# Kernel tuning notes

Hardware: AMD Instinct MI355X
Metric: run time of the kernel (lower is better)

## Reference

```python
import jax, jax.numpy as jnp
import numpy as np

N_NODES = 20000
N_ATTRS = 5000
IN_FEATURES = 512
OUT_FEATURES = 128
ALPHA = 0.2  # LeakyReLU negative slope
NEG_INF = -9e15


def setup_inputs() -> dict:
    key = jax.random.key(0)
    k1, k2, k3, k4, k5 = jax.random.split(key, 5)
    node_embedding = jax.random.normal(k1, (N_NODES, IN_FEATURES), dtype=jnp.float32)
    attr_embedding = jax.random.normal(k2, (N_ATTRS, IN_FEATURES), dtype=jnp.float32)
    feat_mat = jax.random.randint(k3, (N_NODES, N_ATTRS), 0, 2, dtype=jnp.int32)
    # xavier_uniform with gain=1.414 (as in torch init)
    gain = 1.414
    lim_W = gain * np.sqrt(6.0 / (IN_FEATURES + OUT_FEATURES))
    W = jax.random.uniform(k4, (IN_FEATURES, OUT_FEATURES), minval=-lim_W, maxval=lim_W, dtype=jnp.float32)
    lim_a = gain * np.sqrt(6.0 / (2 * OUT_FEATURES + 1))
    a = jax.random.uniform(k5, (2 * OUT_FEATURES, 1), minval=-lim_a, maxval=lim_a, dtype=jnp.float32)
    return {"node_embedding": node_embedding, "attr_embedding": attr_embedding,
            "feat_mat": feat_mat, "W": W, "a": a}


def reference(node_embedding, attr_embedding, feat_mat, W, a):
    # Linear projections
    node_h = node_embedding @ W            # [N, F]
    attr_h = attr_embedding @ W            # [M, F]
    # Additive attention scores: e[i,j] = leakyrelu(a1.node_h[i] + a2.attr_h[j])
    wh1 = node_h @ a[:OUT_FEATURES, :]     # [N, 1]
    wh2 = attr_h @ a[OUT_FEATURES:, :]     # [M, 1]
    e = jax.nn.leaky_relu(wh1 + wh2.T, negative_slope=ALPHA)  # [N, M]
    # Mask where there is no node-attribute link, then softmax over attrs
    attention = jnp.where(feat_mat > 0, e, NEG_INF)
    attention = jax.nn.softmax(attention, axis=1)
    # (dropout is identity in eval mode)
    h_prime = attention @ attr_h           # [N, F]
    return jax.nn.elu(h_prime)             # concat=True branch
```

## Files before the change

kernel.cpp:

```cpp
#include <hip/hip_runtime.h>

#define N_NODES 20000
#define N_ATTRS 5000
#define IN_F    512
#define OUT_F   128
#define KP      5120
#define KSTEPS  (KP / 32)
#define WH2_PAD 5376
#define LOG2E   1.4426950408889634f

typedef _Float16 f16x8 __attribute__((ext_vector_type(8)));
typedef float    f32x4 __attribute__((ext_vector_type(4)));

__device__ __forceinline__ float fast_exp2(float x) {
    return __builtin_amdgcn_exp2f(x);
}

__global__ __launch_bounds__(256) void prep_kernel(
    const float* __restrict__ W, const float* __restrict__ a,
    float* __restrict__ Wa1, float* __restrict__ Wa2, _Float16* __restrict__ Wp) {
    int gt = blockIdx.x * blockDim.x + threadIdx.x;
    if (gt < IN_F) {
        int k = gt;
        float s1 = 0.f, s2 = 0.f;
        for (int f = 0; f < OUT_F; ++f) {
            float w = W[k * OUT_F + f];
            s1 += w * a[f];
            s2 += w * a[OUT_F + f];
        }
        Wa1[k] = s1 * LOG2E;
        Wa2[k] = s2 * LOG2E;
    }
    for (int idx = gt; idx < IN_F * OUT_F; idx += gridDim.x * blockDim.x) {
        int j    = idx & 7;
        int lane = (idx >> 3) & 63;
        int nb   = (idx >> 9) & 7;
        int kb   = idx >> 12;
        int k = kb * 32 + (lane >> 4) * 8 + j;
        int n = nb * 16 + (lane & 15);
        Wp[idx] = (_Float16)W[k * OUT_F + n];
    }
}

__global__ __launch_bounds__(256) void wh_kernel(
    const float* __restrict__ node_emb, const float* __restrict__ attr_emb,
    const float* __restrict__ Wa1, const float* __restrict__ Wa2,
    float* __restrict__ wh1, float* __restrict__ wh2) {
    int wave = threadIdx.x >> 6, lane = threadIdx.x & 63;
    int r = blockIdx.x * 4 + wave;
    const float* src;
    const float* vec;
    float* dst;
    if (r < N_NODES) {
        src = node_emb + (size_t)r * IN_F; vec = Wa1; dst = wh1 + r;
    } else {
        int r2 = r - N_NODES;
        src = attr_emb + (size_t)r2 * IN_F; vec = Wa2; dst = wh2 + r2;
    }
    float4 ra = *reinterpret_cast<const float4*>(src + lane * 8);
    float4 rb = *reinterpret_cast<const float4*>(src + lane * 8 + 4);
    const float* vp = vec + lane * 8;
    float s = ra.x * vp[0] + ra.y * vp[1] + ra.z * vp[2] + ra.w * vp[3]
            + rb.x * vp[4] + rb.y * vp[5] + rb.z * vp[6] + rb.w * vp[7];
#pragma unroll
    for (int off = 1; off < 64; off <<= 1) s += __shfl_xor(s, off, 64);
    if (lane == 0) *dst = s;
}

__global__ __launch_bounds__(256) void max_kernel(
    float* __restrict__ wh2, float* __restrict__ maxp) {
    __shared__ float red[4];
    int t = threadIdx.x;
    float m = -1e30f;
    for (int j = t; j < N_ATTRS; j += 256) m = fmaxf(m, wh2[j]);
    for (int j = N_ATTRS + t; j < WH2_PAD; j += 256) wh2[j] = 0.f;
#pragma unroll
    for (int off = 1; off < 64; off <<= 1) m = fmaxf(m, __shfl_xor(m, off, 64));
    int wave = t >> 6, lane = t & 63;
    if (lane == 0) red[wave] = m;
    __syncthreads();
    if (t == 0) *maxp = fmaxf(fmaxf(red[0], red[1]), fmaxf(red[2], red[3]));
}

__global__ __launch_bounds__(256) void attr_h_kernel(
    const float* __restrict__ attr_emb, const _Float16* __restrict__ Wp,
    _Float16* __restrict__ Vp) {
    int wave = threadIdx.x >> 6, lane = threadIdx.x & 63;
    int m = lane & 15, quad = lane >> 4;
    int j0 = (blockIdx.x * 4 + wave) * 16;
    int j = j0 + m;
    bool valid = j < N_ATTRS;
    f32x4 acc[8];
#pragma unroll
    for (int nb = 0; nb < 8; ++nb)
#pragma unroll
        for (int t = 0; t < 4; ++t) acc[nb][t] = 0.f;
    const float* arow = attr_emb + (size_t)j * IN_F;
    for (int kk = 0; kk < IN_F / 32; ++kk) {
        f16x8 afrag;
        if (valid) {
            float4 ra = *reinterpret_cast<const float4*>(arow + kk * 32 + quad * 8);
            float4 rb = *reinterpret_cast<const float4*>(arow + kk * 32 + quad * 8 + 4);
            afrag[0] = (_Float16)ra.x; afrag[1] = (_Float16)ra.y;
            afrag[2] = (_Float16)ra.z; afrag[3] = (_Float16)ra.w;
            afrag[4] = (_Float16)rb.x; afrag[5] = (_Float16)rb.y;
            afrag[6] = (_Float16)rb.z; afrag[7] = (_Float16)rb.w;
        } else {
#pragma unroll
            for (int t = 0; t < 8; ++t) afrag[t] = (_Float16)0.f;
        }
        const _Float16* wbase = Wp + (size_t)(kk * 8) * 64 * 8;
#pragma unroll
        for (int nb = 0; nb < 8; ++nb) {
            f16x8 bfrag;
            __builtin_memcpy(&bfrag, wbase + (nb * 64 + lane) * 8, 16);
            acc[nb] = __builtin_amdgcn_mfma_f32_16x16x32_f16(afrag, bfrag, acc[nb], 0, 0, 0);
        }
    }
#pragma unroll
    for (int nb = 0; nb < 8; ++nb) {
#pragma unroll
        for (int reg = 0; reg < 4; ++reg) {
            int jr = j0 + quad * 4 + reg;
            int n = nb * 16 + m;
            float v = (jr < N_ATTRS) ? acc[nb][reg] : 0.f;
            size_t idx = ((size_t)((jr >> 5) * 8 + nb) * 64 +
                          (((jr >> 3) & 3) * 16 + m)) * 8 + (jr & 7);
            Vp[idx] = (_Float16)v;
        }
    }
}

__global__ __launch_bounds__(256, 4) void attn_kernel(
    const int* __restrict__ feat, const float* __restrict__ wh1,
    const float* __restrict__ wh2, const float* __restrict__ maxwh2,
    const _Float16* __restrict__ Vp, float* __restrict__ out) {
    __shared__ float accs[16][132];
    __shared__ float rsums[16];

    int wave = threadIdx.x >> 6, lane = threadIdx.x & 63;
    int m = lane & 15, quad = lane >> 4;
    int i0 = blockIdx.x * 16;
    int i = i0 + m;
    float wh1i = wh1[i];
    float emax = wh1i + maxwh2[0];
    float Mi = fmaxf(emax, 0.2f * emax) - 12.f;
    const int* frow = feat + (size_t)i * N_ATTRS;

    f32x4 acc[8];
#pragma unroll
    for (int nb = 0; nb < 8; ++nb)
#pragma unroll
        for (int t = 0; t < 4; ++t) acc[nb][t] = 0.f;
    float s = 0.f;

    int kk0 = wave * (KSTEPS / 4);
    int kk1 = kk0 + (KSTEPS / 4);

    int jb = kk0 * 32 + quad * 8;
    int4 f0 = {0, 0, 0, 0}, f1 = {0, 0, 0, 0};
    if (jb < N_ATTRS) {
        f0 = *reinterpret_cast<const int4*>(frow + jb);
        f1 = *reinterpret_cast<const int4*>(frow + jb + 4);
    }
    float4 w2a = *reinterpret_cast<const float4*>(wh2 + jb);
    float4 w2b = *reinterpret_cast<const float4*>(wh2 + jb + 4);

    const _Float16* vbase = Vp + (size_t)(kk0 * 8) * 64 * 8;

    for (int kk = kk0; kk < kk1; ++kk) {
        int jbn = jb + 32;
        int4 nf0 = {0, 0, 0, 0}, nf1 = {0, 0, 0, 0};
        float4 nw2a = {0.f, 0.f, 0.f, 0.f}, nw2b = {0.f, 0.f, 0.f, 0.f};
        if (kk + 1 < kk1) {
            if (jbn < N_ATTRS) {
                nf0 = *reinterpret_cast<const int4*>(frow + jbn);
                nf1 = *reinterpret_cast<const int4*>(frow + jbn + 4);
            }
            nw2a = *reinterpret_cast<const float4*>(wh2 + jbn);
            nw2b = *reinterpret_cast<const float4*>(wh2 + jbn + 4);
        }

        int   fi[8] = {f0.x, f0.y, f0.z, f0.w, f1.x, f1.y, f1.z, f1.w};
        float w2[8] = {w2a.x, w2a.y, w2a.z, w2a.w, w2b.x, w2b.y, w2b.z, w2b.w};
        f16x8 afrag;
#pragma unroll
        for (int t = 0; t < 8; ++t) {
            float e = wh1i + w2[t];
            float l = fmaxf(e, 0.2f * e);
            float p = fast_exp2(l - Mi);
            p = (fi[t] > 0) ? p : 0.f;
            _Float16 ph = (_Float16)p;
            s += (float)ph;
            afrag[t] = ph;
        }

#pragma unroll
        for (int nb = 0; nb < 8; ++nb) {
            f16x8 bfrag;
            __builtin_memcpy(&bfrag, vbase + (nb * 64 + lane) * 8, 16);
            acc[nb] = __builtin_amdgcn_mfma_f32_16x16x32_f16(afrag, bfrag, acc[nb], 0, 0, 0);
        }

        f0 = nf0; f1 = nf1; w2a = nw2a; w2b = nw2b; jb = jbn;
        vbase += 8 * 64 * 8;
    }

    s += __shfl_xor(s, 16, 64);
    s += __shfl_xor(s, 32, 64);

#pragma unroll
    for (int w = 0; w < 4; ++w) {
        if (wave == w) {
            if (w == 0) {
#pragma unroll
                for (int nb = 0; nb < 8; ++nb)
#pragma unroll
                    for (int reg = 0; reg < 4; ++reg)
                        accs[quad * 4 + reg][nb * 16 + m] = acc[nb][reg];
                if (lane < 16) rsums[lane] = s;
            } else {
#pragma unroll
                for (int nb = 0; nb < 8; ++nb)
#pragma unroll
                    for (int reg = 0; reg < 4; ++reg)
                        accs[quad * 4 + reg][nb * 16 + m] += acc[nb][reg];
                if (lane < 16) rsums[lane] += s;
            }
        }
        __syncthreads();
    }

    for (int o = threadIdx.x; o < 16 * 128; o += 256) {
        int lr = o >> 7, n = o & 127;
        float v = accs[lr][n];
        float rs = rsums[lr];
        rs = (rs > 0.f) ? rs : 1.f;
        float h = v / rs;
        float ov = (h > 0.f) ? h : (fast_exp2(h * LOG2E) - 1.f);
        out[(size_t)(i0 + lr) * OUT_F + n] = ov;
    }
}

extern "C" void kernel_launch(void* const* d_in, const int* in_sizes, int n_in,
                              void* d_out, int out_size, void* d_ws, size_t ws_size,
                              hipStream_t stream) {
    const float* node_emb = (const float*)d_in[0];
    const float* attr_emb = (const float*)d_in[1];
    const int*   feat     = (const int*)d_in[2];
    const float* W        = (const float*)d_in[3];
    const float* a        = (const float*)d_in[4];
    float*       out      = (float*)d_out;

    char* ws = (char*)d_ws;
    float*    Wa1 = (float*)(ws + 0);
    float*    Wa2 = (float*)(ws + 4096);
    float*    wh1 = (float*)(ws + 8192);
    float*    wh2 = (float*)(ws + 90112);
    float*    mx  = (float*)(ws + 111616);
    _Float16* Wp  = (_Float16*)(ws + 131072);
    _Float16* Vp  = (_Float16*)(ws + 262144);

    prep_kernel<<<64, 256, 0, stream>>>(W, a, Wa1, Wa2, Wp);
    wh_kernel<<<6250, 256, 0, stream>>>(node_emb, attr_emb, Wa1, Wa2, wh1, wh2);
    max_kernel<<<1, 256, 0, stream>>>(wh2, mx);
    attr_h_kernel<<<80, 256, 0, stream>>>(attr_emb, Wp, Vp);
    attn_kernel<<<1250, 256, 0, stream>>>(feat, wh1, wh2, mx, Vp, out);
}
```

Measured before the change: 689.5 us.

## Stage attention probabilities through swizzled LDS with coalesced per-row feat loads

Each wave now computes masked softmax numerators for 4 full rows. It reads contiguous 1KB spans of feat_mat per row with nontemporal 16-byte loads, prefetching one chunk ahead. The fp16 probabilities go into a double-buffered, XOR-swizzled LDS tile, and waves then read MFMA A fragments from it for their own K slice. The goal is better-coalesced and deeper in-flight streaming of the dominant feat_mat traffic. In exchange it adds a block barrier per chunk and LDS round trips, and row-sum reductions now use full-wave shuffles.

```diff
diff --git a/kernel.cpp b/kernel.cpp
--- a/kernel.cpp
+++ b/kernel.cpp
@@ -5,12 +5,15 @@
 #define IN_F    512
 #define OUT_F   128
 #define KP      5120
-#define KSTEPS  (KP / 32)
+#define CHUNK   512
+#define NCH     10
+#define KLOC    16
 #define WH2_PAD 5376
 #define LOG2E   1.4426950408889634f
 
 typedef _Float16 f16x8 __attribute__((ext_vector_type(8)));
 typedef float    f32x4 __attribute__((ext_vector_type(4)));
+typedef int      i32x4 __attribute__((ext_vector_type(4)));
 
 __device__ __forceinline__ float fast_exp2(float x) {
     return __builtin_amdgcn_exp2f(x);
@@ -135,80 +138,120 @@
     const int* __restrict__ feat, const float* __restrict__ wh1,
     const float* __restrict__ wh2, const float* __restrict__ maxwh2,
     const _Float16* __restrict__ Vp, float* __restrict__ out) {
-    __shared__ float accs[16][132];
+    __shared__ unsigned int pbuf[2][KLOC * 256];
     __shared__ float rsums[16];
 
     int wave = threadIdx.x >> 6, lane = threadIdx.x & 63;
-    int m = lane & 15, quad = lane >> 4;
     int i0 = blockIdx.x * 16;
-    int i = i0 + m;
-    float wh1i = wh1[i];
-    float emax = wh1i + maxwh2[0];
-    float Mi = fmaxf(emax, 0.2f * emax) - 12.f;
-    const int* frow = feat + (size_t)i * N_ATTRS;
+    int r0 = wave * 4;
+
+    float mw2 = maxwh2[0];
+    float w1[4], Mi[4];
+#pragma unroll
+    for (int rr = 0; rr < 4; ++rr) {
+        float v = wh1[i0 + r0 + rr];
+        w1[rr] = v;
+        float em = v + mw2;
+        Mi[rr] = fmaxf(em, 0.2f * em) - 12.f;
+    }
+    const int* fbase = feat + (size_t)(i0 + r0) * N_ATTRS;
 
     f32x4 acc[8];
 #pragma unroll
     for (int nb = 0; nb < 8; ++nb)
 #pragma unroll
         for (int t = 0; t < 4; ++t) acc[nb][t] = 0.f;
-    float s = 0.f;
-
-    int kk0 = wave * (KSTEPS / 4);
-    int kk1 = kk0 + (KSTEPS / 4);
-
-    int jb = kk0 * 32 + quad * 8;
-    int4 f0 = {0, 0, 0, 0}, f1 = {0, 0, 0, 0};
-    if (jb < N_ATTRS) {
-        f0 = *reinterpret_cast<const int4*>(frow + jb);
-        f1 = *reinterpret_cast<const int4*>(frow + jb + 4);
-    }
-    float4 w2a = *reinterpret_cast<const float4*>(wh2 + jb);
-    float4 w2b = *reinterpret_cast<const float4*>(wh2 + jb + 4);
-
-    const _Float16* vbase = Vp + (size_t)(kk0 * 8) * 64 * 8;
-
-    for (int kk = kk0; kk < kk1; ++kk) {
-        int jbn = jb + 32;
-        int4 nf0 = {0, 0, 0, 0}, nf1 = {0, 0, 0, 0};
-        float4 nw2a = {0.f, 0.f, 0.f, 0.f}, nw2b = {0.f, 0.f, 0.f, 0.f};
-        if (kk + 1 < kk1) {
-            if (jbn < N_ATTRS) {
-                nf0 = *reinterpret_cast<const int4*>(frow + jbn);
-                nf1 = *reinterpret_cast<const int4*>(frow + jbn + 4);
+    float s[4] = {0.f, 0.f, 0.f, 0.f};
+
+    int wK8  = lane >> 3;
+    int wq   = (lane >> 1) & 3;
+    int whh  = lane & 1;
+    int rq = lane >> 4;
+
+    i32x4 fr[4][2];
+#pragma unroll
+    for (int rr = 0; rr < 4; ++rr)
+#pragma unroll
+        for (int t = 0; t < 2; ++t) {
+            int off = t * 256 + 4 * lane;
+            fr[rr][t] = __builtin_nontemporal_load(
+                reinterpret_cast<const i32x4*>(fbase + (size_t)rr * N_ATTRS + off));
+        }
+
+    for (int c = 0; c < NCH; ++c) {
+        char* pw = (char*)pbuf[c & 1];
+        int cb = c * CHUNK;
+
+#pragma unroll
+        for (int rr = 0; rr < 4; ++rr) {
+            int m = r0 + rr;
+#pragma unroll
+            for (int t = 0; t < 2; ++t) {
+                i32x4 f = fr[rr][t];
+                int jg = cb + t * 256 + 4 * lane;
+                float4 w2 = *reinterpret_cast<const float4*>(wh2 + jg);
+                int   fi[4] = {f.x, f.y, f.z, f.w};
+                float wv[4] = {w2.x, w2.y, w2.z, w2.w};
+                union { _Float16 h[4]; uint2 u; } pk;
+#pragma unroll
+                for (int e = 0; e < 4; ++e) {
+                    float ee = w1[rr] + wv[e];
+                    float l = fmaxf(ee, 0.2f * ee);
+                    float p = fast_exp2(l - Mi[rr]);
+                    bool ok = (fi[e] > 0) && (jg + e < N_ATTRS);
+                    p = ok ? p : 0.f;
+                    _Float16 ph = (_Float16)p;
+                    s[rr] += (float)ph;
+                    pk.h[e] = ph;
+                }
+                int K = t * 8 + wK8;
+                int S = (wq + 4 * (K & 1)) * 16;
+                int addr = K * 1024 + (((m * 16 + wq * 256) + whh * 8) ^ S);
+                *reinterpret_cast<uint2*>(pw + addr) = pk.u;
             }
-            nw2a = *reinterpret_cast<const float4*>(wh2 + jbn);
-            nw2b = *reinterpret_cast<const float4*>(wh2 + jbn + 4);
-        }
-
-        int   fi[8] = {f0.x, f0.y, f0.z, f0.w, f1.x, f1.y, f1.z, f1.w};
-        float w2[8] = {w2a.x, w2a.y, w2a.z, w2a.w, w2b.x, w2b.y, w2b.z, w2b.w};
-        f16x8 afrag;
-#pragma unroll
-        for (int t = 0; t < 8; ++t) {
-            float e = wh1i + w2[t];
-            float l = fmaxf(e, 0.2f * e);
-            float p = fast_exp2(l - Mi);
-            p = (fi[t] > 0) ? p : 0.f;
-            _Float16 ph = (_Float16)p;
-            s += (float)ph;
-            afrag[t] = ph;
-        }
-
-#pragma unroll
-        for (int nb = 0; nb < 8; ++nb) {
-            f16x8 bfrag;
-            __builtin_memcpy(&bfrag, vbase + (nb * 64 + lane) * 8, 16);
-            acc[nb] = __builtin_amdgcn_mfma_f32_16x16x32_f16(afrag, bfrag, acc[nb], 0, 0, 0);
-        }
-
-        f0 = nf0; f1 = nf1; w2a = nw2a; w2b = nw2b; jb = jbn;
-        vbase += 8 * 64 * 8;
-    }
-
-    s += __shfl_xor(s, 16, 64);
-    s += __shfl_xor(s, 32, 64);
-
+        }
+
+        __syncthreads();
+
+        {
+            int ncb = (c + 1 < NCH) ? (c + 1) * CHUNK : 0;
+#pragma unroll
+            for (int rr = 0; rr < 4; ++rr)
+#pragma unroll
+                for (int t = 0; t < 2; ++t) {
+                    int off = ncb + t * 256 + 4 * lane;
+                    off = min(off, N_ATTRS - 4);
+                    fr[rr][t] = __builtin_nontemporal_load(
+                        reinterpret_cast<const i32x4*>(fbase + (size_t)rr * N_ATTRS + off));
+                }
+        }
+
+#pragma unroll
+        for (int u = 0; u < 4; ++u) {
+            int Kl = wave * 4 + u;
+            int S = (rq + 4 * (Kl & 1)) * 16;
+            f16x8 afrag;
+            __builtin_memcpy(&afrag, pw + Kl * 1024 + ((lane * 16) ^ S), 16);
+            const _Float16* vb = Vp + (size_t)(c * KLOC + Kl) * 4096;
+#pragma unroll
+            for (int nb = 0; nb < 8; ++nb) {
+                f16x8 bfrag;
+                __builtin_memcpy(&bfrag, vb + nb * 512 + lane * 8, 16);
+                acc[nb] = __builtin_amdgcn_mfma_f32_16x16x32_f16(afrag, bfrag, acc[nb], 0, 0, 0);
+            }
+        }
+    }
+
+#pragma unroll
+    for (int rr = 0; rr < 4; ++rr) {
+        float v = s[rr];
+#pragma unroll
+        for (int off = 1; off < 64; off <<= 1) v += __shfl_xor(v, off, 64);
+        if (lane == 0) rsums[r0 + rr] = v;
+    }
+
+    float* accp = (float*)pbuf;
+    int m16 = lane & 15, quad = lane >> 4;
 #pragma unroll
     for (int w = 0; w < 4; ++w) {
         if (wave == w) {
@@ -217,15 +260,13 @@
                 for (int nb = 0; nb < 8; ++nb)
 #pragma unroll
                     for (int reg = 0; reg < 4; ++reg)
-                        accs[quad * 4 + reg][nb * 16 + m] = acc[nb][reg];
-                if (lane < 16) rsums[lane] = s;
+                        accp[(quad * 4 + reg) * 128 + nb * 16 + m16] = acc[nb][reg];
             } else {
 #pragma unroll
                 for (int nb = 0; nb < 8; ++nb)
 #pragma unroll
                     for (int reg = 0; reg < 4; ++reg)
-                        accs[quad * 4 + reg][nb * 16 + m] += acc[nb][reg];
-                if (lane < 16) rsums[lane] += s;
+                        accp[(quad * 4 + reg) * 128 + nb * 16 + m16] += acc[nb][reg];
             }
         }
         __syncthreads();
@@ -233,7 +274,7 @@
 
     for (int o = threadIdx.x; o < 16 * 128; o += 256) {
         int lr = o >> 7, n = o & 127;
-        float v = accs[lr][n];
+        float v = accp[lr * 128 + n];
         float rs = rsums[lr];
         rs = (rs > 0.f) ? rs : 1.f;
         float h = v / rs;
```

New measurement: 720.3 us. +4.5%, slower.
